# Kernel optimization log

Hardware: AMD Instinct MI355X
Metric: run time of the kernel (lower is better)

Reference implementation:

```python
import jax, jax.numpy as jnp
import numpy as np

K = 3        # kernel size (square)
PAD = 1
STRIDE = 1


def conv2d(x, w, b, stride=STRIDE, pad=PAD):
    out = jax.lax.conv_general_dilated(
        x, w, (stride, stride), [(pad, pad), (pad, pad)],
        dimension_numbers=('NCHW', 'OIHW', 'NCHW'))
    return out + b[None, :, None, None]


def deform_sample(x, offset, mask):
    """Bilinear sampling at learned offsets (torchvision deform_conv2d v2 semantics).
    x: (B,C,H,W); offset: (B,2*K*K,Ho,Wo) as (dy,dx) pairs per kernel tap;
    mask: (B,K*K,Ho,Wo) already sigmoided. Returns (B,C,K*K,Ho,Wo)."""
    B, C, H, W = x.shape
    KK = mask.shape[1]
    Ho, Wo = offset.shape[2], offset.shape[3]
    off = offset.reshape(B, KK, 2, Ho, Wo)
    dy, dx = off[:, :, 0], off[:, :, 1]                      # (B,KK,Ho,Wo)
    ky, kx = jnp.meshgrid(jnp.arange(K), jnp.arange(K), indexing='ij')
    ky = ky.reshape(-1).astype(x.dtype)                       # (KK,)
    kx = kx.reshape(-1).astype(x.dtype)
    base_y = (jnp.arange(Ho) * STRIDE - PAD).astype(x.dtype)  # (Ho,)
    base_x = (jnp.arange(Wo) * STRIDE - PAD).astype(x.dtype)
    py = base_y[None, None, :, None] + ky[None, :, None, None] + dy
    px = base_x[None, None, None, :] + kx[None, :, None, None] + dx
    y0 = jnp.floor(py)
    x0 = jnp.floor(px)
    wy1 = py - y0; wx1 = px - x0
    wy0 = 1.0 - wy1; wx0 = 1.0 - wx1

    def gather(yi, xi):
        # zero-padded bilinear corner gather -> (B,C,KK,Ho,Wo)
        valid = ((yi >= 0) & (yi < H) & (xi >= 0) & (xi < W)).astype(x.dtype)
        yc = jnp.clip(yi, 0, H - 1).astype(jnp.int32)
        xc = jnp.clip(xi, 0, W - 1).astype(jnp.int32)
        vals = jax.vmap(lambda xb, yb, xib: xb[:, yb, xib])(x, yc, xc)
        return vals * valid[:, None]

    samp = (gather(y0, x0) * (wy0 * wx0)[:, None]
            + gather(y0, x0 + 1.0) * (wy0 * wx1)[:, None]
            + gather(y0 + 1.0, x0) * (wy1 * wx0)[:, None]
            + gather(y0 + 1.0, x0 + 1.0) * (wy1 * wx1)[:, None])
    return samp * mask[:, None]


def setup_inputs() -> dict:
    key = jax.random.key(0)
    k = jax.random.split(key, 8)
    B, Cin, Cout, H, W = 4, 256, 256, 64, 64
    stdv = 1.0 / np.sqrt(Cin * K * K)
    x = jax.random.normal(k[0], (B, Cin, H, W), dtype=jnp.float32)
    weight = jax.random.uniform(k[1], (Cout, Cin, K, K), minval=-stdv, maxval=stdv, dtype=jnp.float32)
    bias = jnp.zeros((Cout,), dtype=jnp.float32)
    # offset/mask convs are zero-init in the original; use small random values
    # so the irregular-sampling path is actually exercised.
    off_w = jax.random.normal(k[2], (2 * K * K, Cin, K, K), dtype=jnp.float32) * 0.01
    off_b = jax.random.normal(k[3], (2 * K * K,), dtype=jnp.float32) * 0.5
    mask_w = jax.random.normal(k[4], (K * K, Cin, K, K), dtype=jnp.float32) * 0.01
    mask_b = jax.random.normal(k[5], (K * K,), dtype=jnp.float32) * 0.1
    return {"x": x, "weight": weight, "bias": bias,
            "off_w": off_w, "off_b": off_b, "mask_w": mask_w, "mask_b": mask_b}


def reference(x, weight, bias, off_w, off_b, mask_w, mask_b):
    offset = conv2d(x, off_w, off_b)                      # (B,2*KK,H,W)
    mask = jax.nn.sigmoid(conv2d(x, mask_w, mask_b))      # (B,KK,H,W)
    samp = deform_sample(x, offset, mask)                 # (B,C,KK,H,W)
    O, C = weight.shape[0], weight.shape[1]
    out = jnp.einsum('bckhw,ock->bohw', samp, weight.reshape(O, C, K * K))
    return out + bias[None, :, None, None]
```

## Files before the change

kernel.cpp:

```cpp
#include <hip/hip_runtime.h>
#include <hip/hip_bf16.h>
#include <string.h>


typedef __attribute__((ext_vector_type(8))) short short8;
typedef __attribute__((ext_vector_type(8))) _Float16 half8;
typedef __attribute__((ext_vector_type(16))) float floatx16;

__device__ __forceinline__ unsigned bfbits(float f) {
    unsigned u;
    __builtin_memcpy(&u, &f, 4);
    return (u + 0x7fffu + ((u >> 16) & 1u)) >> 16;
}
__device__ __forceinline__ unsigned pack_bf16(float lo, float hi) {
    return bfbits(lo) | (bfbits(hi) << 16);
}
__device__ __forceinline__ unsigned pack_f16(float lo, float hi) {
    _Float16 a = (_Float16)lo, b = (_Float16)hi;
    unsigned short ua, ub;
    __builtin_memcpy(&ua, &a, 2);
    __builtin_memcpy(&ub, &b, 2);
    return (unsigned)ua | ((unsigned)ub << 16);
}

__device__ __forceinline__ void gl_lds4(const float* g, float* l) {
    __builtin_amdgcn_global_load_lds(
        (const __attribute__((address_space(1))) unsigned int*)g,
        (__attribute__((address_space(3))) unsigned int*)l,
        4, 0, 0);
}

__global__ __launch_bounds__(256) void xpose_hwc_kernel(
    const float* __restrict__ x, unsigned short* __restrict__ xt)
{
    __shared__ float stage[256 * 65];
    const int bid = blockIdx.x;
    const int b = bid >> 6, y = bid & 63;
    const int tid = threadIdx.x;
    const float* src = x + (size_t)b * 256 * 4096 + y * 64;

#pragma unroll
    for (int i = 0; i < 16; ++i) {
        int idx = i * 256 + tid;
        int c = idx >> 4, xq = idx & 15;
        float4 v = *(const float4*)&src[(size_t)c * 4096 + xq * 4];
        stage[c * 65 + xq * 4 + 0] = v.x;
        stage[c * 65 + xq * 4 + 1] = v.y;
        stage[c * 65 + xq * 4 + 2] = v.z;
        stage[c * 65 + xq * 4 + 3] = v.w;
    }
    __syncthreads();

    unsigned short* dst = xt + (size_t)bid * 16384;
#pragma unroll
    for (int i = 0; i < 32; ++i) {
        int c2 = (tid & 127) * 2;
        int xx = i * 2 + (tid >> 7);
        float f0 = stage[c2 * 65 + xx];
        float f1 = stage[(c2 + 1) * 65 + xx];
        *(unsigned*)&dst[xx * 256 + c2] = pack_f16(f0, f1);
    }
}

__global__ __launch_bounds__(256) void weight_pack_kernel(
    const float* __restrict__ w, const float* __restrict__ off_w,
    const float* __restrict__ mask_w,
    unsigned short* __restrict__ ws_b, unsigned short* __restrict__ ws_a2)
{
    __shared__ float slab[32 * 289];
    const int bid = blockIdx.x;
    const int tid = threadIdx.x;

    if (bid < 64) {
        const int nt = bid >> 3, cb = bid & 7;
        const float* wbase = w + (size_t)nt * 32 * 2304 + cb * 288;
#pragma unroll
        for (int i = 0; i < 9; ++i) {
            int idx = i * 256 + tid;
            int o = idx / 72, f4 = idx % 72;
            float4 v = *(const float4*)&wbase[(size_t)o * 2304 + f4 * 4];
            slab[o * 289 + f4 * 4 + 0] = v.x;
            slab[o * 289 + f4 * 4 + 1] = v.y;
            slab[o * 289 + f4 * 4 + 2] = v.z;
            slab[o * 289 + f4 * 4 + 3] = v.w;
        }
        __syncthreads();
#pragma unroll
        for (int pass = 0; pass < 5; ++pass) {
            int rid = pass * 8 + (tid >> 5);
            if (rid < 36) {
                int kk = rid >> 2, q = rid & 3;
                int no = tid & 31;
                unsigned pk[4];
#pragma unroll
                for (int i = 0; i < 4; ++i) {
                    float f0 = slab[no * 289 + (q * 8 + 2 * i) * 9 + kk];
                    float f1 = slab[no * 289 + (q * 8 + 2 * i + 1) * 9 + kk];
                    pk[i] = pack_bf16(f0, f1);
                }
                size_t u = ((size_t)nt * 288 + kk * 32 + cb * 4 + q) * 32 + no;
                *(uint4*)&ws_b[u * 8] = make_uint4(pk[0], pk[1], pk[2], pk[3]);
            }
        }
    } else {
        int e = (bid - 64) * 256 + tid;
        int lan = e & 31;
        int ku = e >> 5;
        int kk = ku >> 5;
        int c0 = (ku & 31) * 8;
        int o = lan;
        float f[8];
#pragma unroll
        for (int j = 0; j < 8; ++j) {
            int c = c0 + j;
            float v = 0.f;
            if (o < 18)      v = off_w[((size_t)o * 256 + c) * 9 + kk];
            else if (o < 27) v = mask_w[((size_t)(o - 18) * 256 + c) * 9 + kk];
            f[j] = v;
        }
        unsigned pk[4];
#pragma unroll
        for (int i = 0; i < 4; ++i) pk[i] = pack_f16(f[2 * i], f[2 * i + 1]);
        *(uint4*)&ws_a2[(size_t)e * 8] = make_uint4(pk[0], pk[1], pk[2], pk[3]);
    }
}

__global__ __launch_bounds__(512) void offmask_mfma_kernel(
    const float* __restrict__ x, const unsigned short* __restrict__ ws_a2,
    const float* __restrict__ off_b, const float* __restrict__ mask_b,
    float* __restrict__ ws_off)
{
    __shared__ float stage[256 * 64];
    __shared__ uint4 bufB[2][2048];
    const int bid = blockIdx.x;
    const int row = (bid & 7) * 32 + (bid >> 3);
    const int b = row >> 6, ho = row & 63;
    const int tid = threadIdx.x;
    const int l = tid & 63;
    const int w = tid >> 6;
    const int lan = l & 31, h = l >> 5;
    const float* xb = x + (size_t)b * 256 * 4096;

    floatx16 acc;
#pragma unroll
    for (int r = 0; r < 16; ++r) acc[r] = 0.f;

    const int n = l;
    const int ku0 = w;
    const int ntile = w >> 2, kq = w & 3;

    auto stage_row = [&](int hh) {
        if (hh >= 0 && hh < 64) {
            const float* src = xb + hh * 64;
#pragma unroll
            for (int i = 0; i < 32; ++i) {
                int c = w * 32 + i;
                gl_lds4(src + (size_t)c * 4096 + l, &stage[c * 64]);
            }
        } else {
#pragma unroll
            for (int i = 0; i < 32; ++i) {
                int c = w * 32 + i;
                stage[c * 64 + l] = 0.f;
            }
        }
    };

    auto build = [&](int kk, int kx) {
        int px = n - 1 + kx;
        bool vx = (px >= 0 && px < 64);
        int pxc = vx ? px : 0;
        int buf = kk & 1;
#pragma unroll
        for (int j = 0; j < 4; ++j) {
            int ku = ku0 + 8 * j;
            int c0 = ku * 8;
            float v[8];
#pragma unroll
            for (int jj = 0; jj < 8; ++jj) {
                float t = stage[(c0 + jj) * 64 + pxc];
                v[jj] = vx ? t : 0.f;
            }
            unsigned pk[4];
#pragma unroll
            for (int i = 0; i < 4; ++i) pk[i] = pack_f16(v[2 * i], v[2 * i + 1]);
            bufB[buf][ku * 64 + n] = make_uint4(pk[0], pk[1], pk[2], pk[3]);
        }
    };

    auto domfma = [&](int kk) {
        int buf = kk & 1;
        const uint4* a4 = (const uint4*)ws_a2;
#pragma unroll
        for (int s4 = 0; s4 < 4; ++s4) {
            int s = kq * 4 + s4;
            int kul = s * 2 + h;
            uint4 ua = a4[(size_t)(kk * 32 + kul) * 32 + lan];
            uint4 ub = bufB[buf][kul * 64 + ntile * 32 + lan];
            half8 a, bb;
            __builtin_memcpy(&a, &ua, 16);
            __builtin_memcpy(&bb, &ub, 16);
            acc = __builtin_amdgcn_mfma_f32_32x32x16_f16(a, bb, acc, 0, 0, 0);
        }
    };

    for (int ky = 0; ky < 3; ++ky) {
        __syncthreads();
        stage_row(ho - 1 + ky);
        __syncthreads();
#pragma unroll
        for (int kx = 0; kx < 3; ++kx) {
            int kk = ky * 3 + kx;
            build(kk, kx);
            __syncthreads();
            domfma(kk);
        }
    }
    __syncthreads();

    float* red = (float*)bufB;
#pragma unroll
    for (int r = 0; r < 16; ++r) red[(w * 64 + l) * 16 + r] = acc[r];
    __syncthreads();
    for (int idx = tid; idx < 27 * 64; idx += 512) {
        int oc = idx >> 6, wo = idx & 63;
        int nt2 = wo >> 5, nn = wo & 31;
        int h2 = (oc >> 2) & 1;
        int r = (oc & 3) | ((oc >> 3) << 2);
        int lane2 = nn + 32 * h2;
        float s = 0.f;
#pragma unroll
        for (int kq2 = 0; kq2 < 4; ++kq2)
            s += red[((nt2 * 4 + kq2) * 64 + lane2) * 16 + r];
        float v;
        if (oc < 18) {
            v = s + off_b[oc];
        } else {
            float t = s + mask_b[oc - 18];
            v = 1.f / (1.f + expf(-t));
        }
        ws_off[(size_t)row * 1728 + idx] = v;
    }
}

__global__ __launch_bounds__(512) void deform_gemm_kernel(
    const unsigned short* __restrict__ xt, const float* __restrict__ ws_off,
    const unsigned short* __restrict__ ws_b, const float* __restrict__ bias,
    float* __restrict__ out)
{
    __shared__ float params[576 * 8];
    __shared__ float biasl[256];
    __shared__ uint4 tile[2][2048];

    const int bid = blockIdx.x;
    const int row = (bid & 7) * 32 + (bid >> 3);
    const int b = row >> 6, ho = row & 63;
    const int tid = threadIdx.x;
    const int l = tid & 63;
    const int wid = tid >> 6;
    const int lan = l & 31;
    const int h = l >> 5;

    if (tid < 256) biasl[tid] = bias[tid];

    {
        const float* ob = ws_off + (size_t)row * 1728;
        for (int it = tid; it < 576; it += 512) {
            int kk = it >> 6, p = it & 63;
            float dy = ob[(2 * kk) * 64 + p];
            float dx = ob[(2 * kk + 1) * 64 + p];
            float mk = ob[(18 + kk) * 64 + p];
            int ky = kk / 3, kx = kk - ky * 3;
            float py = (float)(ho - 1 + ky) + dy;
            float px = (float)(p - 1 + kx) + dx;
            float y0f = floorf(py), x0f = floorf(px);
            float wy1 = py - y0f, wx1 = px - x0f;
            float wy0 = 1.f - wy1, wx0 = 1.f - wx1;
            int y0 = (int)y0f, xi0 = (int)x0f;
            int y1 = y0 + 1, xi1 = xi0 + 1;
            float vy0 = (y0 >= 0 && y0 < 64) ? 1.f : 0.f;
            float vy1 = (y1 >= 0 && y1 < 64) ? 1.f : 0.f;
            float vx0 = (xi0 >= 0 && xi0 < 64) ? 1.f : 0.f;
            float vx1 = (xi1 >= 0 && xi1 < 64) ? 1.f : 0.f;
            float wr0 = wy0 * vy0 * mk, wr1 = wy1 * vy1 * mk;
            float wa = wx0 * vx0, wb2 = wx1 * vx1;
            int yc0 = min(max(y0, 0), 63), yc1 = min(max(y1, 0), 63);
            int xc0 = min(max(xi0, 0), 63), xc1 = min(max(xi1, 0), 63);
            float* pr = &params[it * 8];
            pr[0] = wr0 * wa;  pr[1] = wr0 * wb2;
            pr[2] = wr1 * wa;  pr[3] = wr1 * wb2;
            pr[4] = __int_as_float((yc0 * 64 + xc0) << 9);
            pr[5] = __int_as_float((yc0 * 64 + xc1) << 9);
            pr[6] = __int_as_float((yc1 * 64 + xc0) << 9);
            pr[7] = __int_as_float((yc1 * 64 + xc1) << 9);
        }
    }
    __syncthreads();

    const char* xb16 = (const char*)xt + ((size_t)b << 21);
    const uint4* wb4 = (const uint4*)ws_b;

    floatx16 acc0, acc1;
#pragma unroll
    for (int r = 0; r < 16; ++r) { acc0[r] = 0.f; acc1[r] = 0.f; }

    uint4 gA[2][4], gB[2][4];
    float4 wvA[2], wvB[2];
    uint4 ua[16];

    auto issue_half = [&](int kk, int i0, uint4 (&g)[2][4], float4 (&wv)[2]) {
#pragma unroll
        for (int i = 0; i < 2; ++i) {
            int p = wid * 8 + 2 * (i0 + i) + h;
            const float* pr = &params[(kk * 64 + p) * 8];
            __builtin_memcpy(&wv[i], pr, 16);
            int4 ov;
            __builtin_memcpy(&ov, pr + 4, 16);
            __builtin_memcpy(&g[i][0], xb16 + ov.x + (lan << 4), 16);
            __builtin_memcpy(&g[i][1], xb16 + ov.y + (lan << 4), 16);
            __builtin_memcpy(&g[i][2], xb16 + ov.z + (lan << 4), 16);
            __builtin_memcpy(&g[i][3], xb16 + ov.w + (lan << 4), 16);
        }
    };

    auto pack_half = [&](int buf, int i0, uint4 (&g)[2][4], float4 (&wv)[2]) {
        char* tb = (char*)&tile[buf][0];
#pragma unroll
        for (int i = 0; i < 2; ++i) {
            int p = wid * 8 + 2 * (i0 + i) + h;
            half8 h00, h01, h10, h11;
            __builtin_memcpy(&h00, &g[i][0], 16);
            __builtin_memcpy(&h01, &g[i][1], 16);
            __builtin_memcpy(&h10, &g[i][2], 16);
            __builtin_memcpy(&h11, &g[i][3], 16);
            unsigned pk[4];
#pragma unroll
            for (int j = 0; j < 4; ++j) {
                float v0 = wv[i].x * (float)h00[2 * j]     + wv[i].y * (float)h01[2 * j]
                         + wv[i].z * (float)h10[2 * j]     + wv[i].w * (float)h11[2 * j];
                float v1 = wv[i].x * (float)h00[2 * j + 1] + wv[i].y * (float)h01[2 * j + 1]
                         + wv[i].z * (float)h10[2 * j + 1] + wv[i].w * (float)h11[2 * j + 1];
                pk[j] = pack_bf16(v0, v1);
            }
            uint4 wv4 = make_uint4(pk[0], pk[1], pk[2], pk[3]);
            __builtin_memcpy(tb + lan * 1024 + ((p << 4) ^ (lan << 4)), &wv4, 16);
        }
    };

    issue_half(0, 0, gA, wvA);
    pack_half(0, 0, gA, wvA);
    issue_half(0, 2, gB, wvB);
    pack_half(0, 2, gB, wvB);
    __syncthreads();

    for (int kk = 0; kk < 9; ++kk) {
        const int buf = kk & 1, nbuf = (kk + 1) & 1;

#pragma unroll
        for (int ks = 0; ks < 16; ++ks) {
            int kul = ks * 2 + h;
            ua[ks] = wb4[((size_t)wid * 288 + kk * 32 + kul) * 32 + lan];
        }
        if (kk < 8) issue_half(kk + 1, 0, gA, wvA);

        {
            const char* tb = (const char*)&tile[buf][0];
#pragma unroll
            for (int ks = 0; ks < 8; ++ks) {
                int kul = ks * 2 + h;
                uint4 ub0, ub1;
                __builtin_memcpy(&ub0, tb + kul * 1024 + ((lan << 4) ^ (kul << 4)), 16);
                __builtin_memcpy(&ub1, tb + kul * 1024 + (((32 + lan) << 4) ^ (kul << 4)), 16);
                short8 a, b0, b1;
                __builtin_memcpy(&a, &ua[ks], 16);
                __builtin_memcpy(&b0, &ub0, 16);
                __builtin_memcpy(&b1, &ub1, 16);
                acc0 = __builtin_amdgcn_mfma_f32_32x32x16_bf16(a, b0, acc0, 0, 0, 0);
                acc1 = __builtin_amdgcn_mfma_f32_32x32x16_bf16(a, b1, acc1, 0, 0, 0);
            }
        }

        if (kk < 8) {
            pack_half(nbuf, 0, gA, wvA);
            issue_half(kk + 1, 2, gB, wvB);
        }

        {
            const char* tb = (const char*)&tile[buf][0];
#pragma unroll
            for (int ks = 8; ks < 16; ++ks) {
                int kul = ks * 2 + h;
                uint4 ub0, ub1;
                __builtin_memcpy(&ub0, tb + kul * 1024 + ((lan << 4) ^ (kul << 4)), 16);
                __builtin_memcpy(&ub1, tb + kul * 1024 + (((32 + lan) << 4) ^ (kul << 4)), 16);
                short8 a, b0, b1;
                __builtin_memcpy(&a, &ua[ks], 16);
                __builtin_memcpy(&b0, &ub0, 16);
                __builtin_memcpy(&b1, &ub1, 16);
                acc0 = __builtin_amdgcn_mfma_f32_32x32x16_bf16(a, b0, acc0, 0, 0, 0);
                acc1 = __builtin_amdgcn_mfma_f32_32x32x16_bf16(a, b1, acc1, 0, 0, 0);
            }
        }

        if (kk < 8) pack_half(nbuf, 2, gB, wvB);
        __syncthreads();
    }

#pragma unroll
    for (int nt = 0; nt < 2; ++nt) {
#pragma unroll
        for (int r = 0; r < 16; ++r) {
            int o = wid * 32 + (r & 3) + 8 * (r >> 2) + 4 * h;
            int woo = nt * 32 + lan;
            float v = (nt == 0) ? acc0[r] : acc1[r];
            out[(((size_t)b * 256 + o) * 64 + ho) * 64 + woo] = v + biasl[o];
        }
    }
}

extern "C" void kernel_launch(void* const* d_in, const int* in_sizes, int n_in,
                              void* d_out, int out_size, void* d_ws, size_t ws_size,
                              hipStream_t stream) {
    const float* x      = (const float*)d_in[0];
    const float* weight = (const float*)d_in[1];
    const float* bias   = (const float*)d_in[2];
    const float* off_w  = (const float*)d_in[3];
    const float* off_b  = (const float*)d_in[4];
    const float* mask_w = (const float*)d_in[5];
    const float* mask_b = (const float*)d_in[6];
    float* out = (float*)d_out;

    float* ws_off = (float*)d_ws;
    unsigned short* ws_b  = (unsigned short*)((char*)d_ws + 1769472);
    unsigned short* ws_a2 = (unsigned short*)((char*)d_ws + 2949120);
    unsigned short* xt    = (unsigned short*)((char*)d_ws + 3096576);

    hipLaunchKernelGGL(weight_pack_kernel, dim3(100), dim3(256), 0, stream,
                       weight, off_w, mask_w, ws_b, ws_a2);
    hipLaunchKernelGGL(xpose_hwc_kernel, dim3(256), dim3(256), 0, stream,
                       x, xt);
    hipLaunchKernelGGL(offmask_mfma_kernel, dim3(256), dim3(512), 0, stream,
                       x, ws_a2, off_b, mask_b, ws_off);
    hipLaunchKernelGGL(deform_gemm_kernel, dim3(256), dim3(512), 0, stream,
                       xt, ws_off, ws_b, bias, out);
}
```

Measured before the change: 139.9 us.

## Feed offset/mask conv from transposed f16 HWC input via swizzled 16-byte LDS loads

The offset/mask convolution kernel now reads the already-transposed half-precision HWC copy of x instead of the fp32 NCHW input. It stages all three input rows at once into XOR-swizzled LDS using 16-byte global-to-LDS loads, with zero-padded borders. This removes the per-tap repacking step and most block barriers. The cost is a dependency on the transpose kernel's output layout, and the whole staging buffer is loaded before any MFMA work starts, so loads no longer overlap with compute.

```diff
diff --git a/kernel.cpp b/kernel.cpp
--- a/kernel.cpp
+++ b/kernel.cpp
@@ -23,11 +23,11 @@
     return (unsigned)ua | ((unsigned)ub << 16);
 }
 
-__device__ __forceinline__ void gl_lds4(const float* g, float* l) {
+__device__ __forceinline__ void gl_lds16(const void* g, void* l) {
     __builtin_amdgcn_global_load_lds(
         (const __attribute__((address_space(1))) unsigned int*)g,
         (__attribute__((address_space(3))) unsigned int*)l,
-        4, 0, 0);
+        16, 0, 0);
 }
 
 __global__ __launch_bounds__(256) void xpose_hwc_kernel(
@@ -126,12 +126,11 @@
 }
 
 __global__ __launch_bounds__(512) void offmask_mfma_kernel(
-    const float* __restrict__ x, const unsigned short* __restrict__ ws_a2,
+    const unsigned short* __restrict__ xt, const unsigned short* __restrict__ ws_a2,
     const float* __restrict__ off_b, const float* __restrict__ mask_b,
     float* __restrict__ ws_off)
 {
-    __shared__ float stage[256 * 64];
-    __shared__ uint4 bufB[2][2048];
+    __shared__ uint4 stage[3 * 66 * 32];
     const int bid = blockIdx.x;
     const int row = (bid & 7) * 32 + (bid >> 3);
     const int b = row >> 6, ho = row & 63;
@@ -139,86 +138,62 @@
     const int l = tid & 63;
     const int w = tid >> 6;
     const int lan = l & 31, h = l >> 5;
-    const float* xb = x + (size_t)b * 256 * 4096;
+    const int ntile = w >> 2, kq = w & 3;
+
+    const char* xtb = (const char*)xt + (size_t)b * 64 * 32768;
+    for (int r = 0; r < 3; ++r) {
+        int y = ho - 1 + r;
+        uint4* rowbase = &stage[r * 66 * 32];
+        if (y >= 0 && y < 64) {
+            const char* src = xtb + (size_t)y * 32768;
+#pragma unroll
+            for (int i = 0; i < 4; ++i) {
+                int g0 = 32 + (w * 4 + i) * 64;
+                int g = g0 + l;
+                int p01 = g >> 5, j = g & 31;
+                int kul = j ^ (p01 & 7);
+                gl_lds16(src + ((size_t)(p01 - 1) * 32 + kul) * 16,
+                         rowbase + g0);
+            }
+            if (tid < 64) {
+                int g = (tid < 32) ? tid : (2080 + (tid - 32));
+                rowbase[g] = make_uint4(0, 0, 0, 0);
+            }
+        } else {
+            for (int g = tid; g < 2112; g += 512)
+                rowbase[g] = make_uint4(0, 0, 0, 0);
+        }
+    }
+    __syncthreads();
 
     floatx16 acc;
 #pragma unroll
     for (int r = 0; r < 16; ++r) acc[r] = 0.f;
 
-    const int n = l;
-    const int ku0 = w;
-    const int ntile = w >> 2, kq = w & 3;
-
-    auto stage_row = [&](int hh) {
-        if (hh >= 0 && hh < 64) {
-            const float* src = xb + hh * 64;
-#pragma unroll
-            for (int i = 0; i < 32; ++i) {
-                int c = w * 32 + i;
-                gl_lds4(src + (size_t)c * 4096 + l, &stage[c * 64]);
-            }
-        } else {
-#pragma unroll
-            for (int i = 0; i < 32; ++i) {
-                int c = w * 32 + i;
-                stage[c * 64 + l] = 0.f;
-            }
-        }
-    };
-
-    auto build = [&](int kk, int kx) {
-        int px = n - 1 + kx;
-        bool vx = (px >= 0 && px < 64);
-        int pxc = vx ? px : 0;
-        int buf = kk & 1;
-#pragma unroll
-        for (int j = 0; j < 4; ++j) {
-            int ku = ku0 + 8 * j;
-            int c0 = ku * 8;
-            float v[8];
-#pragma unroll
-            for (int jj = 0; jj < 8; ++jj) {
-                float t = stage[(c0 + jj) * 64 + pxc];
-                v[jj] = vx ? t : 0.f;
-            }
-            unsigned pk[4];
-#pragma unroll
-            for (int i = 0; i < 4; ++i) pk[i] = pack_f16(v[2 * i], v[2 * i + 1]);
-            bufB[buf][ku * 64 + n] = make_uint4(pk[0], pk[1], pk[2], pk[3]);
-        }
-    };
-
-    auto domfma = [&](int kk) {
-        int buf = kk & 1;
-        const uint4* a4 = (const uint4*)ws_a2;
-#pragma unroll
-        for (int s4 = 0; s4 < 4; ++s4) {
-            int s = kq * 4 + s4;
-            int kul = s * 2 + h;
-            uint4 ua = a4[(size_t)(kk * 32 + kul) * 32 + lan];
-            uint4 ub = bufB[buf][kul * 64 + ntile * 32 + lan];
-            half8 a, bb;
-            __builtin_memcpy(&a, &ua, 16);
-            __builtin_memcpy(&bb, &ub, 16);
-            acc = __builtin_amdgcn_mfma_f32_32x32x16_f16(a, bb, acc, 0, 0, 0);
-        }
-    };
-
+    const uint4* a4 = (const uint4*)ws_a2;
+    const int n = ntile * 32 + lan;
+#pragma unroll
     for (int ky = 0; ky < 3; ++ky) {
-        __syncthreads();
-        stage_row(ho - 1 + ky);
-        __syncthreads();
 #pragma unroll
         for (int kx = 0; kx < 3; ++kx) {
             int kk = ky * 3 + kx;
-            build(kk, kx);
-            __syncthreads();
-            domfma(kk);
-        }
-    }
-    __syncthreads();
-
-    float* red = (float*)bufB;
+            int p01 = n + kx;
+#pragma unroll
+            for (int s4 = 0; s4 < 4; ++s4) {
+                int s = kq * 4 + s4;
+                int kul = s * 2 + h;
+                uint4 ua = a4[(size_t)(kk * 32 + kul) * 32 + lan];
+                uint4 ub = stage[(ky * 66 + p01) * 32 + (kul ^ (p01 & 7))];
+                half8 a, bb;
+                __builtin_memcpy(&a, &ua, 16);
+                __builtin_memcpy(&bb, &ub, 16);
+                acc = __builtin_amdgcn_mfma_f32_32x32x16_f16(a, bb, acc, 0, 0, 0);
+            }
+        }
+    }
+    __syncthreads();
+
+    float* red = (float*)stage;
 #pragma unroll
     for (int r = 0; r < 16; ++r) red[(w * 64 + l) * 16 + r] = acc[r];
     __syncthreads();
@@ -440,7 +415,7 @@
     hipLaunchKernelGGL(xpose_hwc_kernel, dim3(256), dim3(256), 0, stream,
                        x, xt);
     hipLaunchKernelGGL(offmask_mfma_kernel, dim3(256), dim3(512), 0, stream,
-                       x, ws_a2, off_b, mask_b, ws_off);
+                       xt, ws_a2, off_b, mask_b, ws_off);
     hipLaunchKernelGGL(deform_gemm_kernel, dim3(256), dim3(512), 0, stream,
                        xt, ws_off, ws_b, bias, out);
 }
```

Result: faster. 132.3 us (-5.4%).
